# Optimization experiments

Hardware: AMD Instinct MI355X
Metric: run time of the kernel (lower is better)

The kernel has to match this reference:

```python
import jax, jax.numpy as jnp
import numpy as np

D_MODEL = 1024
N_HEAD = 16
D_HEAD = D_MODEL // N_HEAD
EXP = 4
B, T = 2, 2048
EPS = 1e-5

def setup_inputs() -> dict:
    key = jax.random.key(0)
    ks = jax.random.split(key, 16)
    s = 0.02
    return {
        "x": jax.random.normal(ks[0], (B, T, D_MODEL), jnp.float32),
        "ln1_w": jnp.ones((D_MODEL,), jnp.float32),
        "ln1_b": jnp.zeros((D_MODEL,), jnp.float32),
        "attn_w": jax.random.normal(ks[1], (D_MODEL, 3 * D_MODEL), jnp.float32) * s,
        "attn_b": jnp.zeros((3 * D_MODEL,), jnp.float32),
        "proj_w": jax.random.normal(ks[2], (D_MODEL, D_MODEL), jnp.float32) * s,
        "proj_b": jnp.zeros((D_MODEL,), jnp.float32),
        "ln2_w": jnp.ones((D_MODEL,), jnp.float32),
        "ln2_b": jnp.zeros((D_MODEL,), jnp.float32),
        "fc_w": jax.random.normal(ks[3], (D_MODEL, EXP * D_MODEL), jnp.float32) * s,
        "fc_b": jnp.zeros((EXP * D_MODEL,), jnp.float32),
        "fc2_w": jax.random.normal(ks[4], (EXP * D_MODEL, D_MODEL), jnp.float32) * s,
        "fc2_b": jnp.zeros((D_MODEL,), jnp.float32),
    }

def _layernorm(x, w, b):
    mu = jnp.mean(x, axis=-1, keepdims=True)
    var = jnp.mean(jnp.square(x - mu), axis=-1, keepdims=True)
    return (x - mu) * jax.lax.rsqrt(var + EPS) * w + b

def _attn(x, attn_w, attn_b, proj_w, proj_b):
    Bx, Tx, C = x.shape
    qkv = x @ attn_w + attn_b  # [B,T,3C]
    q, k, v = jnp.split(qkv, 3, axis=-1)
    # [B, H, T, Dh]
    q = q.reshape(Bx, Tx, N_HEAD, D_HEAD).transpose(0, 2, 1, 3)
    k = k.reshape(Bx, Tx, N_HEAD, D_HEAD).transpose(0, 2, 1, 3)
    v = v.reshape(Bx, Tx, N_HEAD, D_HEAD).transpose(0, 2, 1, 3)
    att = jnp.einsum('bhqd,bhkd->bhqk', q, k) * (1.0 / np.sqrt(D_HEAD))
    causal = jnp.tril(jnp.ones((Tx, Tx), bool))
    att = jnp.where(causal, att, -jnp.inf)
    att = jax.nn.softmax(att, axis=-1)
    y = jnp.einsum('bhqk,bhkd->bhqd', att, v)
    y = y.transpose(0, 2, 1, 3).reshape(Bx, Tx, C)
    return y @ proj_w + proj_b

def reference(x, ln1_w, ln1_b, attn_w, attn_b, proj_w, proj_b,
              ln2_w, ln2_b, fc_w, fc_b, fc2_w, fc2_b):
    x = x + _attn(_layernorm(x, ln1_w, ln1_b), attn_w, attn_b, proj_w, proj_b)
    h = _layernorm(x, ln2_w, ln2_b)
    h = jax.nn.gelu(h @ fc_w + fc_b, approximate=False)  # exact GELU (torch nn.GELU default)
    x = x + (h @ fc2_w + fc2_b)
    return x
```

## Files before the change

### kernel.cpp

```cpp
#include <hip/hip_runtime.h>
#include <hip/hip_bf16.h>
#include <math.h>


#define D_MODEL 1024
#define N_HEAD  16
#define D_HEAD  64
#define SEQ_T   2048
#define BATCH   2
#define NROWS   (BATCH * SEQ_T)
#define C3      (3 * D_MODEL)
#define D_FF    (4 * D_MODEL)

typedef __bf16 bf16x8 __attribute__((ext_vector_type(8)));
typedef float  f32x4  __attribute__((ext_vector_type(4)));

#define WAIT_VM6() __builtin_amdgcn_s_waitcnt(0x0F76)
#define WAIT_VM4() __builtin_amdgcn_s_waitcnt(0x0F74)
#define WAIT_VM0() __builtin_amdgcn_s_waitcnt(0x0F70)

__global__ __launch_bounds__(256) void ln_kernel(
    const float* __restrict__ in, const float* __restrict__ w,
    const float* __restrict__ b, __hip_bfloat16* __restrict__ out, int D)
{
    const int row = blockIdx.x;
    const int tid = threadIdx.x;
    const float* x = in + (size_t)row * D;

    float s = 0.f, s2 = 0.f;
    for (int i = tid; i < D; i += 256) {
        float v = x[i];
        s += v; s2 += v * v;
    }
    __shared__ float rs[256], rs2[256];
    rs[tid] = s; rs2[tid] = s2;
    __syncthreads();
    for (int off = 128; off > 0; off >>= 1) {
        if (tid < off) { rs[tid] += rs[tid + off]; rs2[tid] += rs2[tid + off]; }
        __syncthreads();
    }
    const float mu   = rs[0] / D;
    const float var  = rs2[0] / D - mu * mu;
    const float rstd = rsqrtf(var + 1e-5f);

    __hip_bfloat16* o = out + (size_t)row * D;
    for (int i = tid; i < D; i += 256)
        o[i] = __float2bfloat16((x[i] - mu) * rstd * w[i] + b[i]);
}

__global__ __launch_bounds__(256) void transpose_all_kernel(
    const float* __restrict__ attn_w, const float* __restrict__ proj_w,
    const float* __restrict__ fc_w,   const float* __restrict__ fc2_w,
    __hip_bfloat16* __restrict__ attn_wt, __hip_bfloat16* __restrict__ proj_wt,
    __hip_bfloat16* __restrict__ fc_wt,   __hip_bfloat16* __restrict__ fc2_wt)
{
    __shared__ float t[32][33];
    int tb = blockIdx.x;
    const float* W; __hip_bfloat16* Wt; int K, N;
    if (tb < 3072)      { W = attn_w; Wt = attn_wt; K = D_MODEL; N = C3; }
    else if (tb < 4096) { tb -= 3072; W = proj_w; Wt = proj_wt; K = D_MODEL; N = D_MODEL; }
    else if (tb < 8192) { tb -= 4096; W = fc_w;   Wt = fc_wt;   K = D_MODEL; N = D_FF; }
    else                { tb -= 8192; W = fc2_w;  Wt = fc2_wt;  K = D_FF;    N = D_MODEL; }
    const int ntx = N >> 5;
    const int k0 = (tb / ntx) * 32;
    const int n0 = (tb % ntx) * 32;

    const int tx = threadIdx.x & 31;
    const int ty = threadIdx.x >> 5;
#pragma unroll
    for (int i = 0; i < 4; ++i)
        t[ty + 8 * i][tx] = W[(size_t)(k0 + ty + 8 * i) * N + n0 + tx];
    __syncthreads();
#pragma unroll
    for (int i = 0; i < 4; ++i)
        Wt[(size_t)(n0 + ty + 8 * i) * K + k0 + tx] =
            __float2bfloat16(t[tx][ty + 8 * i]);
}

__device__ __forceinline__ void async16(const __hip_bfloat16* g, __hip_bfloat16* l)
{
    __builtin_amdgcn_global_load_lds(
        (const __attribute__((address_space(1))) void*)g,
        (__attribute__((address_space(3))) void*)l, 16, 0, 0);
}

__device__ __forceinline__ float gelu_exact(float v)
{
    return 0.5f * v * (1.0f + erff(v * 0.70710678118654752f));
}

__device__ __forceinline__ void swizzle_bxy(int& bx, int& by)
{
    const int nbx = gridDim.x;
    const int lin = blockIdx.y * nbx + blockIdx.x;
    const int stripe = 4 * nbx;
    const int s = lin / stripe;
    const int rem = lin - s * stripe;
    by = s * 4 + (rem & 3);
    bx = rem >> 2;
}

__device__ __forceinline__ void gemm_pipeline_core(
    const __hip_bfloat16* __restrict__ A,
    const __hip_bfloat16* __restrict__ Bt,
    int K, int row0, int col0,
    int wm, int wn, int ln15, int lq,
    f32x4 (&acc)[4][4])
{
    __shared__ __align__(16) __hip_bfloat16 As0[4096], As1[4096],
                                            As2[4096], As3[4096];
    __shared__ __align__(16) __hip_bfloat16 Bs0[4096], Bs1[4096],
                                            Bs2[4096], Bs3[4096];
    __hip_bfloat16* const Ab[4] = {As0, As1, As2, As3};
    __hip_bfloat16* const Bb[4] = {Bs0, Bs1, Bs2, Bs3};

    const int tid  = threadIdx.x;
    const int wv   = tid >> 6;
    const int lane = tid & 63;
    const int sr = wv * 16 + (lane >> 2);
    const int sq = (lane & 3) * 8;

    auto stage = [&](int kt, __hip_bfloat16* as, __hip_bfloat16* bs) {
        const int k0 = kt * 32;
#pragma unroll
        for (int i = 0; i < 2; ++i) {
            const int r = i * 64 + sr;
            async16(A  + (size_t)(row0 + r) * K + k0 + sq, as + r * 32);
            async16(Bt + (size_t)(col0 + r) * K + k0 + sq, bs + r * 32);
        }
    };

#pragma unroll
    for (int i = 0; i < 4; ++i)
#pragma unroll
        for (int j = 0; j < 4; ++j) acc[i][j] = (f32x4){0.f, 0.f, 0.f, 0.f};

    stage(0, Ab[0], Bb[0]);
    stage(1, Ab[1], Bb[1]);

    const int nt = K >> 5;
    for (int t0 = 0; t0 < nt; t0 += 4) {
#pragma unroll
        for (int u = 0; u < 4; ++u) {
            const int t = t0 + u;
            if (t + 1 < nt) WAIT_VM4(); else WAIT_VM0();
            __builtin_amdgcn_s_barrier();
            const __hip_bfloat16* as = Ab[u];
            const __hip_bfloat16* bs = Bb[u];
            bf16x8 af[4], bfr[4];
#pragma unroll
            for (int mi = 0; mi < 4; ++mi)
                af[mi] = *(const bf16x8*)&as[(wm + mi * 16 + ln15) * 32 + lq * 8];
#pragma unroll
            for (int ni = 0; ni < 4; ++ni)
                bfr[ni] = *(const bf16x8*)&bs[(wn + ni * 16 + ln15) * 32 + lq * 8];
#pragma unroll
            for (int mi = 0; mi < 4; ++mi)
#pragma unroll
                for (int ni = 0; ni < 4; ++ni)
                    acc[mi][ni] = __builtin_amdgcn_mfma_f32_16x16x32_bf16(
                        af[mi], bfr[ni], acc[mi][ni], 0, 0, 0);
            if (t + 2 < nt) stage(t + 2, Ab[(u + 2) & 3], Bb[(u + 2) & 3]);
        }
    }
}

__device__ __forceinline__ void gemm_pipeline_wide(
    const __hip_bfloat16* __restrict__ A,
    const __hip_bfloat16* __restrict__ Bt,
    int K, int row0, int col0,
    int wm, int wn, int ln15, int lq,
    f32x4 (&acc)[8][4])
{
    __shared__ __align__(16) __hip_bfloat16 As0[256 * 32], As1[256 * 32];
    __shared__ __align__(16) __hip_bfloat16 Bs0[128 * 32], Bs1[128 * 32];

    const int tid  = threadIdx.x;
    const int wv   = tid >> 6;
    const int lane = tid & 63;
    const int sr = wv * 16 + (lane >> 2);
    const int sq = (lane & 3) * 8;

    auto stage = [&](int kt, __hip_bfloat16* as, __hip_bfloat16* bs) {
        const int k0 = kt * 32;
#pragma unroll
        for (int i = 0; i < 4; ++i) {
            const int r = i * 64 + sr;
            async16(A + (size_t)(row0 + r) * K + k0 + sq, as + r * 32);
        }
#pragma unroll
        for (int i = 0; i < 2; ++i) {
            const int r = i * 64 + sr;
            async16(Bt + (size_t)(col0 + r) * K + k0 + sq, bs + r * 32);
        }
    };

#pragma unroll
    for (int i = 0; i < 8; ++i)
#pragma unroll
        for (int j = 0; j < 4; ++j) acc[i][j] = (f32x4){0.f, 0.f, 0.f, 0.f};

    stage(0, As0, Bs0);
    stage(1, As1, Bs1);

    const int nt = K >> 5;
    for (int t0 = 0; t0 < nt; t0 += 2) {
#pragma unroll
        for (int u = 0; u < 2; ++u) {
            const int t = t0 + u;
            if (t + 1 < nt) WAIT_VM6(); else WAIT_VM0();
            __builtin_amdgcn_s_barrier();
            const __hip_bfloat16* as = u ? As1 : As0;
            const __hip_bfloat16* bs = u ? Bs1 : Bs0;
            bf16x8 af[8], bfr[4];
#pragma unroll
            for (int mi = 0; mi < 8; ++mi)
                af[mi] = *(const bf16x8*)&as[(wm + mi * 16 + ln15) * 32 + lq * 8];
#pragma unroll
            for (int ni = 0; ni < 4; ++ni)
                bfr[ni] = *(const bf16x8*)&bs[(wn + ni * 16 + ln15) * 32 + lq * 8];
#pragma unroll
            for (int mi = 0; mi < 8; ++mi)
#pragma unroll
                for (int ni = 0; ni < 4; ++ni)
                    acc[mi][ni] = __builtin_amdgcn_mfma_f32_16x16x32_bf16(
                        af[mi], bfr[ni], acc[mi][ni], 0, 0, 0);
            __builtin_amdgcn_s_barrier();
            if (t + 2 < nt) stage(t + 2, u ? As1 : As0, u ? Bs1 : Bs0);
        }
    }
}

__global__ __launch_bounds__(256) void mfma_gemm_kernel(
    const __hip_bfloat16* __restrict__ A,
    const __hip_bfloat16* __restrict__ Bt,
    const float* __restrict__ bias,
    const float* __restrict__ residual,
    void* __restrict__ Cout,
    int M, int N, int K, int act, int outBf16)
{
    int bx, by;
    swizzle_bxy(bx, by);
    const int tid  = threadIdx.x;
    const int wv   = tid >> 6;
    const int lane = tid & 63;
    const int ln15 = lane & 15;
    const int lq   = lane >> 4;
    const int wm   = (wv >> 1) * 64;
    const int wn   = (wv & 1) * 64;
    const int row0 = by * 128;
    const int col0 = bx * 128;

    f32x4 acc[4][4];
    gemm_pipeline_core(A, Bt, K, row0, col0, wm, wn, ln15, lq, acc);

#pragma unroll
    for (int mi = 0; mi < 4; ++mi) {
#pragma unroll
        for (int ni = 0; ni < 4; ++ni) {
            const int gc = col0 + wn + ni * 16 + ln15;
            const float bv = bias[gc];
#pragma unroll
            for (int r = 0; r < 4; ++r) {
                const int gr = row0 + wm + mi * 16 + lq * 4 + r;
                float v = acc[mi][ni][r] + bv;
                if (act == 1) v = gelu_exact(v);
                if (residual) v += residual[(size_t)gr * N + gc];
                if (outBf16)
                    ((__hip_bfloat16*)Cout)[(size_t)gr * N + gc] = __float2bfloat16(v);
                else
                    ((float*)Cout)[(size_t)gr * N + gc] = v;
            }
        }
    }
}

__global__ __launch_bounds__(256, 2) void mfma_gemm_wide_kernel(
    const __hip_bfloat16* __restrict__ A,
    const __hip_bfloat16* __restrict__ Bt,
    const float* __restrict__ bias,
    void* __restrict__ Cout,
    int M, int N, int K, int act, int outBf16)
{
    int bx, by;
    swizzle_bxy(bx, by);
    const int tid  = threadIdx.x;
    const int wv   = tid >> 6;
    const int lane = tid & 63;
    const int ln15 = lane & 15;
    const int lq   = lane >> 4;
    const int wm   = (wv >> 1) * 128;
    const int wn   = (wv & 1) * 64;
    const int row0 = by * 256;
    const int col0 = bx * 128;

    f32x4 acc[8][4];
    gemm_pipeline_wide(A, Bt, K, row0, col0, wm, wn, ln15, lq, acc);

#pragma unroll
    for (int mi = 0; mi < 8; ++mi) {
#pragma unroll
        for (int ni = 0; ni < 4; ++ni) {
            const int gc = col0 + wn + ni * 16 + ln15;
            const float bv = bias[gc];
#pragma unroll
            for (int r = 0; r < 4; ++r) {
                const int gr = row0 + wm + mi * 16 + lq * 4 + r;
                float v = acc[mi][ni][r] + bv;
                if (act == 1) v = gelu_exact(v);
                if (outBf16)
                    ((__hip_bfloat16*)Cout)[(size_t)gr * N + gc] = __float2bfloat16(v);
                else
                    ((float*)Cout)[(size_t)gr * N + gc] = v;
            }
        }
    }
}

__global__ __launch_bounds__(256, 2) void mfma_qkv_kernel(
    const __hip_bfloat16* __restrict__ A,
    const __hip_bfloat16* __restrict__ Bt,
    const float* __restrict__ bias,
    __hip_bfloat16* __restrict__ Qb,
    __hip_bfloat16* __restrict__ Kb,
    __hip_bfloat16* __restrict__ Vtb)
{
    const int K = D_MODEL;
    int bx, by;
    swizzle_bxy(bx, by);
    const int tid  = threadIdx.x;
    const int wv   = tid >> 6;
    const int lane = tid & 63;
    const int ln15 = lane & 15;
    const int lq   = lane >> 4;
    const int wm   = (wv >> 1) * 128;
    const int wn   = (wv & 1) * 64;
    const int row0 = by * 256;
    const int col0 = bx * 128;

    f32x4 acc[8][4];
    gemm_pipeline_wide(A, Bt, K, row0, col0, wm, wn, ln15, lq, acc);

#pragma unroll
    for (int mi = 0; mi < 8; ++mi) {
        const int gr0 = row0 + wm + mi * 16 + lq * 4;
        const int bb  = gr0 >> 11;
        const int q0  = gr0 & 2047;
#pragma unroll
        for (int ni = 0; ni < 4; ++ni) {
            const int gc  = col0 + wn + ni * 16 + ln15;
            const float bv = bias[gc];
            const int sec = gc >> 10;
            const int hd  = (gc & 1023) >> 6;
            const int d   = gc & 63;
            if (sec == 2) {
                unsigned short u[4];
#pragma unroll
                for (int r = 0; r < 4; ++r) {
                    __hip_bfloat16 e = __float2bfloat16(acc[mi][ni][r] + bv);
                    u[r] = *(unsigned short*)&e;
                }
                uint2 pk;
                pk.x = (unsigned int)u[0] | ((unsigned int)u[1] << 16);
                pk.y = (unsigned int)u[2] | ((unsigned int)u[3] << 16);
                *(uint2*)(Vtb + ((size_t)((bb * N_HEAD + hd) * D_HEAD + d)) * SEQ_T + q0) = pk;
            } else {
                __hip_bfloat16* dst = (sec == 0 ? Qb : Kb)
                    + ((size_t)((bb * N_HEAD + hd) * SEQ_T + q0)) * D_HEAD + d;
#pragma unroll
                for (int r = 0; r < 4; ++r)
                    dst[(size_t)r * D_HEAD] = __float2bfloat16(acc[mi][ni][r] + bv);
            }
        }
    }
}

#define ATQ 64
#define ATK 128
#define NQT (SEQ_T / ATQ)
#define KP  72
#define VP  136

__global__ __launch_bounds__(256) void mfma_attn_kernel(
    const __hip_bfloat16* __restrict__ Qb,
    const __hip_bfloat16* __restrict__ Kb,
    const __hip_bfloat16* __restrict__ Vtb,
    __hip_bfloat16* __restrict__ y)
{
    __shared__ __align__(16) __hip_bfloat16 Ks[ATK * KP];
    __shared__ __align__(16) __hip_bfloat16 Vts[D_HEAD * VP];
    __shared__ __align__(16) __hip_bfloat16 Ps[ATQ * VP];

    const int pair = blockIdx.x;
    const int h    = blockIdx.y;
    const int b    = blockIdx.z;
    const int tid  = threadIdx.x;
    const int wv   = tid >> 6;
    const int lane = tid & 63;
    const int ln15 = lane & 15;
    const int lq   = lane >> 4;

    const __hip_bfloat16* Qh = Qb  + (size_t)(b * N_HEAD + h) * SEQ_T * D_HEAD;
    const __hip_bfloat16* Kh = Kb  + (size_t)(b * N_HEAD + h) * SEQ_T * D_HEAD;
    const __hip_bfloat16* Vh = Vtb + (size_t)(b * N_HEAD + h) * D_HEAD * SEQ_T;
    const size_t bT = (size_t)b * SEQ_T;

#pragma unroll 1
    for (int half = 0; half < 2; ++half) {
        const int qt    = half == 0 ? pair : (NQT - 1 - pair);
        const int qbase = qt * ATQ;
        const int ntk   = (qt >> 1) + 1;
        const int qg    = qbase + wv * 16 + ln15;

        bf16x8 qf[2];
#pragma unroll
        for (int kc = 0; kc < 2; ++kc)
            qf[kc] = *(const bf16x8*)(Qh + (size_t)(qbase + wv * 16 + ln15) * D_HEAD
                                      + kc * 32 + lq * 8);

        f32x4 Oacc[4];
#pragma unroll
        for (int dn = 0; dn < 4; ++dn) Oacc[dn] = (f32x4){0.f, 0.f, 0.f, 0.f};
        float m_run = -INFINITY, l_run = 0.f;

        for (int t = 0; t < ntk; ++t) {
            const int kb = t * ATK;
            __syncthreads();
#pragma unroll
            for (int i = 0; i < 4; ++i) {
                const int ch = tid + i * 256;
                const int r = ch >> 3, c8 = (ch & 7) * 8;
                *(bf16x8*)&Ks[r * KP + c8] =
                    *(const bf16x8*)(Kh + (size_t)(kb + r) * D_HEAD + c8);
            }
#pragma unroll
            for (int i = 0; i < 4; ++i) {
                const int ch = tid + i * 256;
                const int r = ch >> 4, c8 = (ch & 15) * 8;
                *(bf16x8*)&Vts[r * VP + c8] =
                    *(const bf16x8*)(Vh + (size_t)r * SEQ_T + kb + c8);
            }
            __syncthreads();

            f32x4 st[8];
#pragma unroll
            for (int jf = 0; jf < 8; ++jf) st[jf] = (f32x4){0.f, 0.f, 0.f, 0.f};
#pragma unroll
            for (int jf = 0; jf < 8; ++jf) {
                const bf16x8 kf0 = *(const bf16x8*)&Ks[(jf * 16 + ln15) * KP + lq * 8];
                const bf16x8 kf1 = *(const bf16x8*)&Ks[(jf * 16 + ln15) * KP + 32 + lq * 8];
                st[jf] = __builtin_amdgcn_mfma_f32_16x16x32_bf16(kf0, qf[0], st[jf], 0, 0, 0);
                st[jf] = __builtin_amdgcn_mfma_f32_16x16x32_bf16(kf1, qf[1], st[jf], 0, 0, 0);
            }

            const bool last = (t == ntk - 1);
#pragma unroll
            for (int jf = 0; jf < 8; ++jf)
#pragma unroll
                for (int r = 0; r < 4; ++r) {
                    float v = st[jf][r] * 0.125f;
                    if (last && (kb + jf * 16 + lq * 4 + r) > qg) v = -INFINITY;
                    st[jf][r] = v;
                }

            float tmax = st[0][0];
#pragma unroll
            for (int jf = 0; jf < 8; ++jf)
#pragma unroll
                for (int r = 0; r < 4; ++r) tmax = fmaxf(tmax, st[jf][r]);
            tmax = fmaxf(tmax, __shfl_xor(tmax, 16));
            tmax = fmaxf(tmax, __shfl_xor(tmax, 32));
            const float mnew  = fmaxf(m_run, tmax);
            const float alpha = __expf(m_run - mnew);
            float psum = 0.f;
#pragma unroll
            for (int jf = 0; jf < 8; ++jf)
#pragma unroll
                for (int r = 0; r < 4; ++r) {
                    const float p = __expf(st[jf][r] - mnew);
                    st[jf][r] = p;
                    psum += p;
                }
            psum += __shfl_xor(psum, 16);
            psum += __shfl_xor(psum, 32);
            l_run = alpha * l_run + psum;
            m_run = mnew;

            float a4[4];
#pragma unroll
            for (int r = 0; r < 4; ++r) a4[r] = __shfl(alpha, lq * 4 + r);
#pragma unroll
            for (int dn = 0; dn < 4; ++dn)
#pragma unroll
                for (int r = 0; r < 4; ++r) Oacc[dn][r] *= a4[r];

#pragma unroll
            for (int jf = 0; jf < 8; ++jf) {
                __hip_bfloat162 p01 = __float22bfloat162_rn(make_float2(st[jf][0], st[jf][1]));
                __hip_bfloat162 p23 = __float22bfloat162_rn(make_float2(st[jf][2], st[jf][3]));
                uint2 pk;
                pk.x = *(unsigned int*)&p01;
                pk.y = *(unsigned int*)&p23;
                *(uint2*)&Ps[(wv * 16 + ln15) * VP + jf * 16 + lq * 4] = pk;
            }

            bf16x8 pf[4];
#pragma unroll
            for (int jc = 0; jc < 4; ++jc)
                pf[jc] = *(const bf16x8*)&Ps[(wv * 16 + ln15) * VP + jc * 32 + lq * 8];
#pragma unroll
            for (int dn = 0; dn < 4; ++dn) {
#pragma unroll
                for (int jc = 0; jc < 4; ++jc) {
                    const bf16x8 vf = *(const bf16x8*)&Vts[(dn * 16 + ln15) * VP + jc * 32 + lq * 8];
                    Oacc[dn] = __builtin_amdgcn_mfma_f32_16x16x32_bf16(
                        pf[jc], vf, Oacc[dn], 0, 0, 0);
                }
            }
        }

        float il[4];
#pragma unroll
        for (int r = 0; r < 4; ++r) il[r] = 1.0f / __shfl(l_run, lq * 4 + r);
#pragma unroll
        for (int dn = 0; dn < 4; ++dn)
#pragma unroll
            for (int r = 0; r < 4; ++r)
                Ps[(wv * 16 + lq * 4 + r) * VP + dn * 16 + ln15] =
                    __float2bfloat16(Oacc[dn][r] * il[r]);
        const int r2 = lane >> 3, c8 = (lane & 7) * 8;
#pragma unroll
        for (int i = 0; i < 2; ++i) {
            const int row = wv * 16 + r2 + 8 * i;
            const bf16x8 val = *(const bf16x8*)&Ps[row * VP + c8];
            *(bf16x8*)(y + (bT + qbase + row) * D_MODEL + h * D_HEAD + c8) = val;
        }
    }
}

extern "C" void kernel_launch(void* const* d_in, const int* in_sizes, int n_in,
                              void* d_out, int out_size, void* d_ws, size_t ws_size,
                              hipStream_t stream)
{
    const float* x      = (const float*)d_in[0];
    const float* ln1_w  = (const float*)d_in[1];
    const float* ln1_b  = (const float*)d_in[2];
    const float* attn_w = (const float*)d_in[3];
    const float* attn_b = (const float*)d_in[4];
    const float* proj_w = (const float*)d_in[5];
    const float* proj_b = (const float*)d_in[6];
    const float* ln2_w  = (const float*)d_in[7];
    const float* ln2_b  = (const float*)d_in[8];
    const float* fc_w   = (const float*)d_in[9];
    const float* fc_b   = (const float*)d_in[10];
    const float* fc2_w  = (const float*)d_in[11];
    const float* fc2_b  = (const float*)d_in[12];
    float* out = (float*)d_out;

    char* ws = (char*)d_ws;
    __hip_bfloat16* Qb      = (__hip_bfloat16*)(ws);
    __hip_bfloat16* Kb      = (__hip_bfloat16*)(ws + (size_t)8  * 1024 * 1024);
    __hip_bfloat16* Vtb     = (__hip_bfloat16*)(ws + (size_t)16 * 1024 * 1024);
    __hip_bfloat16* h_bf    = (__hip_bfloat16*)(ws);
    __hip_bfloat16* ln_buf  = (__hip_bfloat16*)(ws + (size_t)32 * 1024 * 1024);
    __hip_bfloat16* y_buf   = (__hip_bfloat16*)(ws + (size_t)40 * 1024 * 1024);
    float*          xmid    = (float*)(ws + (size_t)48 * 1024 * 1024);
    __hip_bfloat16* attn_wt = (__hip_bfloat16*)(ws + (size_t)64 * 1024 * 1024);
    __hip_bfloat16* proj_wt = (__hip_bfloat16*)(ws + (size_t)70 * 1024 * 1024);
    __hip_bfloat16* fc_wt   = (__hip_bfloat16*)(ws + (size_t)72 * 1024 * 1024);
    __hip_bfloat16* fc2_wt  = (__hip_bfloat16*)(ws + (size_t)80 * 1024 * 1024);

    dim3 blk256(256);

    transpose_all_kernel<<<dim3(12288), blk256, 0, stream>>>(
        attn_w, proj_w, fc_w, fc2_w, attn_wt, proj_wt, fc_wt, fc2_wt);

    ln_kernel<<<dim3(NROWS), blk256, 0, stream>>>(x, ln1_w, ln1_b, ln_buf, D_MODEL);

    mfma_qkv_kernel<<<dim3(C3 / 128, NROWS / 256), blk256, 0, stream>>>(
        ln_buf, attn_wt, attn_b, Qb, Kb, Vtb);

    mfma_attn_kernel<<<dim3(NQT / 2, N_HEAD, BATCH), blk256, 0, stream>>>(
        Qb, Kb, Vtb, y_buf);

    mfma_gemm_kernel<<<dim3(D_MODEL / 128, NROWS / 128), blk256, 0, stream>>>(
        y_buf, proj_wt, proj_b, x, xmid, NROWS, D_MODEL, D_MODEL, 0, 0);

    ln_kernel<<<dim3(NROWS), blk256, 0, stream>>>(xmid, ln2_w, ln2_b, ln_buf, D_MODEL);

    mfma_gemm_wide_kernel<<<dim3(D_FF / 128, NROWS / 256), blk256, 0, stream>>>(
        ln_buf, fc_wt, fc_b, h_bf, NROWS, D_FF, D_MODEL, 1, 1);

    mfma_gemm_kernel<<<dim3(D_MODEL / 128, NROWS / 128), blk256, 0, stream>>>(
        h_bf, fc2_wt, fc2_b, xmid, out, NROWS, D_MODEL, D_FF, 0, 0);
}
```

Baseline: 417.9 us.

## Prefetch K/V tiles into registers and feed P to PV MFMA directly

The attention kernel now issues the global loads for the next K/V tile into registers before computing on the current tile, writing them to LDS after the compute. This overlaps global memory latency with MFMA work. It also drops the P staging buffer in LDS, feeding the softmax probabilities straight from the S accumulator layout into 16x16x16 bf16 MFMAs. The scale is folded into an exp2 with a fused multiply-add. The trade-off is more registers for the prefetch, smaller-K MFMAs, and one extra barrier per tile.

```diff
diff --git a/kernel.cpp b/kernel.cpp
--- a/kernel.cpp
+++ b/kernel.cpp
@@ -13,11 +13,23 @@
 #define D_FF    (4 * D_MODEL)
 
 typedef __bf16 bf16x8 __attribute__((ext_vector_type(8)));
+typedef __bf16 bf16x4t __attribute__((ext_vector_type(4)));
+typedef short  s16x4  __attribute__((ext_vector_type(4)));
 typedef float  f32x4  __attribute__((ext_vector_type(4)));
 
 #define WAIT_VM6() __builtin_amdgcn_s_waitcnt(0x0F76)
 #define WAIT_VM4() __builtin_amdgcn_s_waitcnt(0x0F74)
 #define WAIT_VM0() __builtin_amdgcn_s_waitcnt(0x0F70)
+
+__device__ __forceinline__ f32x4 mfma16_bf16(s16x4 a, s16x4 b, f32x4 c)
+{
+#if __has_builtin(__builtin_amdgcn_mfma_f32_16x16x16_bf16)
+    return __builtin_amdgcn_mfma_f32_16x16x16_bf16(
+        __builtin_bit_cast(bf16x4t, a), __builtin_bit_cast(bf16x4t, b), c, 0, 0, 0);
+#else
+    return __builtin_amdgcn_mfma_f32_16x16x16bf16_1k(a, b, c, 0, 0, 0);
+#endif
+}
 
 __global__ __launch_bounds__(256) void ln_kernel(
     const float* __restrict__ in, const float* __restrict__ w,
@@ -389,7 +401,6 @@
 {
     __shared__ __align__(16) __hip_bfloat16 Ks[ATK * KP];
     __shared__ __align__(16) __hip_bfloat16 Vts[D_HEAD * VP];
-    __shared__ __align__(16) __hip_bfloat16 Ps[ATQ * VP];
 
     const int pair = blockIdx.x;
     const int h    = blockIdx.y;
@@ -405,6 +416,8 @@
     const __hip_bfloat16* Vh = Vtb + (size_t)(b * N_HEAD + h) * D_HEAD * SEQ_T;
     const size_t bT = (size_t)b * SEQ_T;
 
+    const float CEXP = 0.18033688011f;
+
 #pragma unroll 1
     for (int half = 0; half < 2; ++half) {
         const int qt    = half == 0 ? pair : (NQT - 1 - pair);
@@ -412,6 +425,8 @@
         const int ntk   = (qt >> 1) + 1;
         const int qg    = qbase + wv * 16 + ln15;
 
+        __syncthreads();
+
         bf16x8 qf[2];
 #pragma unroll
         for (int kc = 0; kc < 2; ++kc)
@@ -423,24 +438,36 @@
         for (int dn = 0; dn < 4; ++dn) Oacc[dn] = (f32x4){0.f, 0.f, 0.f, 0.f};
         float m_run = -INFINITY, l_run = 0.f;
 
+        uint4 kreg[4], vreg[4];
+        auto load_tile = [&](int t) {
+            const int kb = t * ATK;
+#pragma unroll
+            for (int i = 0; i < 4; ++i) {
+                const int ch = tid + i * 256;
+                const int kr = ch >> 3, kc8 = (ch & 7) * 8;
+                kreg[i] = *(const uint4*)(Kh + (size_t)(kb + kr) * D_HEAD + kc8);
+                const int vr = ch >> 4, vc8 = (ch & 15) * 8;
+                vreg[i] = *(const uint4*)(Vh + (size_t)vr * SEQ_T + kb + vc8);
+            }
+        };
+        auto write_tile = [&]() {
+#pragma unroll
+            for (int i = 0; i < 4; ++i) {
+                const int ch = tid + i * 256;
+                const int kr = ch >> 3, kc8 = (ch & 7) * 8;
+                *(uint4*)&Ks[kr * KP + kc8] = kreg[i];
+                const int vr = ch >> 4, vc8 = (ch & 15) * 8;
+                *(uint4*)&Vts[vr * VP + vc8] = vreg[i];
+            }
+        };
+
+        load_tile(0);
+        write_tile();
+        __syncthreads();
+
         for (int t = 0; t < ntk; ++t) {
             const int kb = t * ATK;
-            __syncthreads();
-#pragma unroll
-            for (int i = 0; i < 4; ++i) {
-                const int ch = tid + i * 256;
-                const int r = ch >> 3, c8 = (ch & 7) * 8;
-                *(bf16x8*)&Ks[r * KP + c8] =
-                    *(const bf16x8*)(Kh + (size_t)(kb + r) * D_HEAD + c8);
-            }
-#pragma unroll
-            for (int i = 0; i < 4; ++i) {
-                const int ch = tid + i * 256;
-                const int r = ch >> 4, c8 = (ch & 15) * 8;
-                *(bf16x8*)&Vts[r * VP + c8] =
-                    *(const bf16x8*)(Vh + (size_t)r * SEQ_T + kb + c8);
-            }
-            __syncthreads();
+            if (t + 1 < ntk) load_tile(t + 1);
 
             f32x4 st[8];
 #pragma unroll
@@ -453,15 +480,13 @@
                 st[jf] = __builtin_amdgcn_mfma_f32_16x16x32_bf16(kf1, qf[1], st[jf], 0, 0, 0);
             }
 
-            const bool last = (t == ntk - 1);
-#pragma unroll
-            for (int jf = 0; jf < 8; ++jf)
-#pragma unroll
-                for (int r = 0; r < 4; ++r) {
-                    float v = st[jf][r] * 0.125f;
-                    if (last && (kb + jf * 16 + lq * 4 + r) > qg) v = -INFINITY;
-                    st[jf][r] = v;
-                }
+            if (t == ntk - 1) {
+#pragma unroll
+                for (int jf = 0; jf < 8; ++jf)
+#pragma unroll
+                    for (int r = 0; r < 4; ++r)
+                        if ((kb + jf * 16 + lq * 4 + r) > qg) st[jf][r] = -INFINITY;
+            }
 
             float tmax = st[0][0];
 #pragma unroll
@@ -471,13 +496,14 @@
             tmax = fmaxf(tmax, __shfl_xor(tmax, 16));
             tmax = fmaxf(tmax, __shfl_xor(tmax, 32));
             const float mnew  = fmaxf(m_run, tmax);
-            const float alpha = __expf(m_run - mnew);
+            const float alpha = exp2f((m_run - mnew) * CEXP);
+            const float mc    = mnew * CEXP;
             float psum = 0.f;
 #pragma unroll
             for (int jf = 0; jf < 8; ++jf)
 #pragma unroll
                 for (int r = 0; r < 4; ++r) {
-                    const float p = __expf(st[jf][r] - mnew);
+                    const float p = exp2f(fmaf(st[jf][r], CEXP, -mc));
                     st[jf][r] = p;
                     psum += p;
                 }
@@ -496,26 +522,24 @@
 
 #pragma unroll
             for (int jf = 0; jf < 8; ++jf) {
-                __hip_bfloat162 p01 = __float22bfloat162_rn(make_float2(st[jf][0], st[jf][1]));
-                __hip_bfloat162 p23 = __float22bfloat162_rn(make_float2(st[jf][2], st[jf][3]));
-                uint2 pk;
-                pk.x = *(unsigned int*)&p01;
-                pk.y = *(unsigned int*)&p23;
-                *(uint2*)&Ps[(wv * 16 + ln15) * VP + jf * 16 + lq * 4] = pk;
-            }
-
-            bf16x8 pf[4];
-#pragma unroll
-            for (int jc = 0; jc < 4; ++jc)
-                pf[jc] = *(const bf16x8*)&Ps[(wv * 16 + ln15) * VP + jc * 32 + lq * 8];
-#pragma unroll
-            for (int dn = 0; dn < 4; ++dn) {
-#pragma unroll
-                for (int jc = 0; jc < 4; ++jc) {
-                    const bf16x8 vf = *(const bf16x8*)&Vts[(dn * 16 + ln15) * VP + jc * 32 + lq * 8];
-                    Oacc[dn] = __builtin_amdgcn_mfma_f32_16x16x32_bf16(
-                        pf[jc], vf, Oacc[dn], 0, 0, 0);
+                s16x4 pfr;
+#pragma unroll
+                for (int s = 0; s < 4; ++s) {
+                    __hip_bfloat16 e = __float2bfloat16(st[jf][s]);
+                    pfr[s] = __builtin_bit_cast(short, e);
                 }
+#pragma unroll
+                for (int dn = 0; dn < 4; ++dn) {
+                    const s16x4 vfr = *(const s16x4*)&Vts[(dn * 16 + ln15) * VP
+                                                          + jf * 16 + lq * 4];
+                    Oacc[dn] = mfma16_bf16(pfr, vfr, Oacc[dn]);
+                }
+            }
+
+            __syncthreads();
+            if (t + 1 < ntk) {
+                write_tile();
+                __syncthreads();
             }
         }
 
@@ -526,13 +550,13 @@
         for (int dn = 0; dn < 4; ++dn)
 #pragma unroll
             for (int r = 0; r < 4; ++r)
-                Ps[(wv * 16 + lq * 4 + r) * VP + dn * 16 + ln15] =
+                Ks[(wv * 16 + lq * 4 + r) * 72 + dn * 16 + ln15] =
                     __float2bfloat16(Oacc[dn][r] * il[r]);
         const int r2 = lane >> 3, c8 = (lane & 7) * 8;
 #pragma unroll
         for (int i = 0; i < 2; ++i) {
             const int row = wv * 16 + r2 + 8 * i;
-            const bf16x8 val = *(const bf16x8*)&Ps[row * VP + c8];
+            const bf16x8 val = *(const bf16x8*)&Ks[row * 72 + c8];
             *(bf16x8*)(y + (bT + qbase + row) * D_MODEL + h * D_HEAD + c8) = val;
         }
     }
```

New measurement: 449.7 us. 1.08x slower.
